# Kernel optimization log

Measured on AMD Instinct MI355X. Metric: run time of the kernel, lower is better.

The kernel has to match this reference:

```python
import jax, jax.numpy as jnp
import numpy as np

VOCAB, NUM_CLASSES, E, H = 50257, 20, 64, 64
B, T = 128, 2048


def setup_inputs() -> dict:
    key = jax.random.key(0)
    ks = jax.random.split(key, 16)
    s_ih = 1.0 / np.sqrt(H)
    u = lambda k, shape: jax.random.uniform(k, shape, jnp.float32, -s_ih, s_ih)
    return {
        'tokens': jax.random.randint(ks[0], (B, T), 0, VOCAB),
        'emb': jax.random.normal(ks[1], (VOCAB, E), jnp.float32),
        # forward-direction GRU params (PyTorch layout: [3H, *], gate order r,z,n)
        'wih_f': u(ks[2], (3 * H, E)), 'whh_f': u(ks[3], (3 * H, H)),
        'bih_f': u(ks[4], (3 * H,)), 'bhh_f': u(ks[5], (3 * H,)),
        # backward-direction GRU params
        'wih_b': u(ks[6], (3 * H, E)), 'whh_b': u(ks[7], (3 * H, H)),
        'bih_b': u(ks[8], (3 * H,)), 'bhh_b': u(ks[9], (3 * H,)),
        # classifier: Linear(4H -> H), GELU, Linear(H -> C)
        'w1': u(ks[10], (H, 4 * H)), 'b1': u(ks[11], (H,)),
        'w2': u(ks[12], (NUM_CLASSES, H)), 'b2': u(ks[13], (NUM_CLASSES,)),
    }


def _gru_dir(x, wih, whh, bih, bhh):
    # x: [B, T, E] -> outputs [B, T, H]; PyTorch GRU gate math, gates (r, z, n)
    xg = jnp.einsum('bte,ge->tbg', x, wih) + bih  # precompute input projections [T,B,3H]
    h0 = jnp.zeros((x.shape[0], H), x.dtype)

    def step(h, xg_t):
        hg = h @ whh.T + bhh
        xr, xz, xn = jnp.split(xg_t, 3, axis=-1)
        hr, hz, hn = jnp.split(hg, 3, axis=-1)
        r = jax.nn.sigmoid(xr + hr)
        z = jax.nn.sigmoid(xz + hz)
        n = jnp.tanh(xn + r * hn)
        h_new = (1.0 - z) * n + z * h
        return h_new, h_new

    _, hs = jax.lax.scan(step, h0, xg)  # hs: [T, B, H]
    return hs.transpose(1, 0, 2)


def reference(tokens, emb, wih_f, whh_f, bih_f, bhh_f,
              wih_b, whh_b, bih_b, bhh_b, w1, b1, w2, b2):
    x = emb[tokens]  # [B, T, E]
    h_fwd = _gru_dir(x, wih_f, whh_f, bih_f, bhh_f)
    h_bwd = _gru_dir(x[:, ::-1], wih_b, whh_b, bih_b, bhh_b)[:, ::-1]
    encoded = jnp.concatenate([h_fwd, h_bwd], axis=-1)  # [B, T, 2H]
    feats = jnp.concatenate([encoded.mean(axis=1), encoded.max(axis=1)], axis=-1)  # [B, 4H]
    hid = jax.nn.gelu(feats @ w1.T + b1, approximate=False)
    return hid @ w2.T + b2  # [B, C]
```

## Files before the change

### kernel.cpp

```cpp
#include <hip/hip_runtime.h>
#include <hip/hip_bf16.h>
#include <math.h>

#define VOCAB 50257
#define NCLS 20
#define EDIM 64
#define HDIM 64
#define BATCH 128
#define TLEN 2048

typedef float v2f __attribute__((ext_vector_type(2)));

__device__ float g_P[(size_t)2 * VOCAB * 192];
__device__ float g_feats[BATCH * 256];

__device__ __forceinline__ float fast_rcp(float x) { return __builtin_amdgcn_rcpf(x); }

__device__ __forceinline__ float fsigmoid(float x) {
    return fast_rcp(1.f + __expf(-x));
}
__device__ __forceinline__ float ftanh(float x) {
    float e = __expf(2.f * x);
    return 1.f - 2.f * fast_rcp(e + 1.f);
}

__global__ __launch_bounds__(384) void precompute_P(
    const float* __restrict__ emb,
    const float* __restrict__ wih_f, const float* __restrict__ bih_f,
    const float* __restrict__ wih_b, const float* __restrict__ bih_b)
{
    const int t = threadIdx.x;
    const int dir = t / 192;
    const int g = t % 192;
    const float* wih = dir ? wih_b : wih_f;
    const float* bih = dir ? bih_b : bih_f;

    float w[64];
#pragma unroll
    for (int e = 0; e < 64; e += 4) {
        float4 v = *(const float4*)(wih + (size_t)g * 64 + e);
        w[e] = v.x; w[e + 1] = v.y; w[e + 2] = v.z; w[e + 3] = v.w;
    }
    const float bias = bih[g];
    float* Pd = g_P + (size_t)dir * VOCAB * 192;

    for (int v = blockIdx.x; v < VOCAB; v += gridDim.x) {
        const float4* er = (const float4*)(emb + (size_t)v * 64);
        float acc = bias;
#pragma unroll
        for (int e4 = 0; e4 < 16; e4++) {
            float4 x = er[e4];
            acc = fmaf(x.x, w[4 * e4 + 0], acc);
            acc = fmaf(x.y, w[4 * e4 + 1], acc);
            acc = fmaf(x.z, w[4 * e4 + 2], acc);
            acc = fmaf(x.w, w[4 * e4 + 3], acc);
        }
        Pd[(size_t)v * 192 + g] = acc;
    }
}

__global__ __launch_bounds__(64, 1) void gru_seq(
    const int* __restrict__ tokens,
    const float* __restrict__ whh_f, const float* __restrict__ bhh_f,
    const float* __restrict__ whh_b, const float* __restrict__ bhh_b)
{
    const int lane = threadIdx.x;
    const int blk = blockIdx.x;
    const int b = blk >> 1;
    const int dir = blk & 1;
    const float* whh = dir ? whh_b : whh_f;
    const float* bhh = dir ? bhh_b : bhh_f;
    const float* Pd = g_P + (size_t)dir * VOCAB * 192;

    __shared__ __align__(16) float h_lds[64];
    __shared__ int tok_lds[TLEN];

    for (int t = lane; t < TLEN; t += 64) tok_lds[t] = tokens[b * TLEN + t];

    v2f wr[32], wz[32], wn[32];
    {
        const float* pr = whh + (size_t)(0 + lane) * 64;
        const float* pz = whh + (size_t)(64 + lane) * 64;
        const float* pn = whh + (size_t)(128 + lane) * 64;
#pragma unroll
        for (int k = 0; k < 16; k++) {
            float4 a = *(const float4*)(pr + 4 * k);
            wr[2 * k] = (v2f){a.x, a.y}; wr[2 * k + 1] = (v2f){a.z, a.w};
            float4 c = *(const float4*)(pz + 4 * k);
            wz[2 * k] = (v2f){c.x, c.y}; wz[2 * k + 1] = (v2f){c.z, c.w};
            float4 d = *(const float4*)(pn + 4 * k);
            wn[2 * k] = (v2f){d.x, d.y}; wn[2 * k + 1] = (v2f){d.z, d.w};
        }
    }
    const float br = bhh[lane], bz = bhh[64 + lane], bn = bhh[128 + lane];

    h_lds[lane] = 0.f;
    float h = 0.f, sum = 0.f, mx = -INFINITY;
    __syncthreads();

    auto tok_at = [&](int s) -> int {
        int ss = s < TLEN ? s : TLEN - 1;
        return tok_lds[dir ? (TLEN - 1 - ss) : ss];
    };

    float xrA, xzA, xnA, xrB, xzB, xnB, xrC, xzC, xnC;
    {
        const float* r0 = Pd + (size_t)tok_at(0) * 192;
        xrA = r0[lane]; xzA = r0[64 + lane]; xnA = r0[128 + lane];
        const float* r1 = Pd + (size_t)tok_at(1) * 192;
        xrB = r1[lane]; xzB = r1[64 + lane]; xnB = r1[128 + lane];
        const float* r2 = Pd + (size_t)tok_at(2) * 192;
        xrC = r2[lane]; xzC = r2[64 + lane]; xnC = r2[128 + lane];
    }

    for (int s = 0; s < TLEN; s++) {
        const float* rp = Pd + (size_t)tok_at(s + 3) * 192;
        float pxr = rp[lane], pxz = rp[64 + lane], pxn = rp[128 + lane];

        v2f ar0 = {0.f, 0.f}, ar1 = {0.f, 0.f};
        v2f az0 = {0.f, 0.f}, az1 = {0.f, 0.f};
        v2f an0 = {0.f, 0.f}, an1 = {0.f, 0.f};
#pragma unroll
        for (int k = 0; k < 16; k++) {
            float4 h4 = *(const float4*)(h_lds + 4 * k);
            v2f h01 = {h4.x, h4.y}, h23 = {h4.z, h4.w};
            ar0 = __builtin_elementwise_fma(h01, wr[2 * k], ar0);
            az0 = __builtin_elementwise_fma(h01, wz[2 * k], az0);
            an0 = __builtin_elementwise_fma(h01, wn[2 * k], an0);
            ar1 = __builtin_elementwise_fma(h23, wr[2 * k + 1], ar1);
            az1 = __builtin_elementwise_fma(h23, wz[2 * k + 1], az1);
            an1 = __builtin_elementwise_fma(h23, wn[2 * k + 1], an1);
        }
        float hr = (ar0.x + ar0.y) + (ar1.x + ar1.y);
        float hz = (az0.x + az0.y) + (az1.x + az1.y);
        float hn = (an0.x + an0.y) + (an1.x + an1.y);

        float r = fsigmoid(xrA + hr + br);
        float z = fsigmoid(xzA + hz + bz);
        float n = ftanh(xnA + r * (hn + bn));
        h = fmaf(z, h - n, n);
        sum += h;
        mx = fmaxf(mx, h);

        __syncthreads();
        h_lds[lane] = h;
        __syncthreads();

        xrA = xrB; xzA = xzB; xnA = xnB;
        xrB = xrC; xzB = xzC; xnB = xnC;
        xrC = pxr; xzC = pxz; xnC = pxn;
    }

    g_feats[b * 256 + dir * 64 + lane] = sum * (1.f / TLEN);
    g_feats[b * 256 + 128 + dir * 64 + lane] = mx;
}

__global__ __launch_bounds__(64) void classifier(
    const float* __restrict__ w1, const float* __restrict__ b1,
    const float* __restrict__ w2, const float* __restrict__ b2,
    float* __restrict__ out)
{
    const int b = blockIdx.x;
    const int i = threadIdx.x;
    __shared__ float f[256];
    __shared__ float hid[64];
    for (int c = i; c < 256; c += 64) f[c] = g_feats[b * 256 + c];
    __syncthreads();

    float acc = b1[i];
    const float* wrow = w1 + (size_t)i * 256;
#pragma unroll 16
    for (int c = 0; c < 256; c++) acc = fmaf(f[c], wrow[c], acc);
    hid[i] = acc * 0.5f * (1.f + erff(acc * 0.70710678118654752f));
    __syncthreads();

    if (i < NCLS) {
        float o = b2[i];
        const float* w2r = w2 + (size_t)i * 64;
#pragma unroll
        for (int j = 0; j < 64; j++) o = fmaf(hid[j], w2r[j], o);
        out[b * NCLS + i] = o;
    }
}

extern "C" void kernel_launch(void* const* d_in, const int* in_sizes, int n_in,
                              void* d_out, int out_size, void* d_ws, size_t ws_size,
                              hipStream_t stream) {
    const int*   tokens = (const int*)  d_in[0];
    const float* emb    = (const float*)d_in[1];
    const float* wih_f  = (const float*)d_in[2];
    const float* whh_f  = (const float*)d_in[3];
    const float* bih_f  = (const float*)d_in[4];
    const float* bhh_f  = (const float*)d_in[5];
    const float* wih_b  = (const float*)d_in[6];
    const float* whh_b  = (const float*)d_in[7];
    const float* bih_b  = (const float*)d_in[8];
    const float* bhh_b  = (const float*)d_in[9];
    const float* w1     = (const float*)d_in[10];
    const float* b1     = (const float*)d_in[11];
    const float* w2     = (const float*)d_in[12];
    const float* b2     = (const float*)d_in[13];
    float* out = (float*)d_out;

    precompute_P<<<1024, 384, 0, stream>>>(emb, wih_f, bih_f, wih_b, bih_b);
    gru_seq<<<2 * BATCH, 64, 0, stream>>>(tokens, whh_f, bhh_f, whh_b, bhh_b);
    classifier<<<BATCH, 64, 0, stream>>>(w1, b1, w2, b2, out);
}
```

Measured before the change: 1.082 ms.

## Interleave gate projections per lane as float4 and fold hidden biases into table

The precomputed token projection table changes from three separate 64-float gate segments to one float4 per lane holding r, z, n and a pad. Each recurrent step then does a single 16-byte gather instead of three scalar loads. The r and z hidden biases are folded into the table, and the table kernel is restructured so one thread computes all three gates for one lane. The step loop is unrolled by 4 with a 4-deep prefetch, and the h·W dot product uses 8-wide vectors. In exchange the table grows by a third, so the precompute kernel writes more data.

Result: slower. 1.618 ms (+49.4%).

```diff
diff --git a/kernel.cpp b/kernel.cpp
--- a/kernel.cpp
+++ b/kernel.cpp
@@ -1,61 +1,77 @@
 #include <hip/hip_runtime.h>
-#include <hip/hip_bf16.h>
 #include <math.h>
 
 #define VOCAB 50257
 #define NCLS 20
-#define EDIM 64
-#define HDIM 64
 #define BATCH 128
 #define TLEN 2048
 
-typedef float v2f __attribute__((ext_vector_type(2)));
+typedef float v8f __attribute__((ext_vector_type(8)));
 
-__device__ float g_P[(size_t)2 * VOCAB * 192];
+__device__ float g_P[(size_t)2 * VOCAB * 256];
 __device__ float g_feats[BATCH * 256];
 
-__device__ __forceinline__ float fast_rcp(float x) { return __builtin_amdgcn_rcpf(x); }
-
 __device__ __forceinline__ float fsigmoid(float x) {
-    return fast_rcp(1.f + __expf(-x));
+    return __builtin_amdgcn_rcpf(1.f + __expf(-x));
 }
 __device__ __forceinline__ float ftanh(float x) {
     float e = __expf(2.f * x);
-    return 1.f - 2.f * fast_rcp(e + 1.f);
+    return 1.f - 2.f * __builtin_amdgcn_rcpf(e + 1.f);
+}
+__device__ __forceinline__ float hsum8(v8f a) {
+    float s0 = a[0] + a[4], s1 = a[1] + a[5], s2 = a[2] + a[6], s3 = a[3] + a[7];
+    return (s0 + s2) + (s1 + s3);
 }
 
-__global__ __launch_bounds__(384) void precompute_P(
+#define DECL_W8(P, base) \
+    const v8f P##0 = ((const v8f*)(base))[0], P##1 = ((const v8f*)(base))[1], \
+              P##2 = ((const v8f*)(base))[2], P##3 = ((const v8f*)(base))[3], \
+              P##4 = ((const v8f*)(base))[4], P##5 = ((const v8f*)(base))[5], \
+              P##6 = ((const v8f*)(base))[6], P##7 = ((const v8f*)(base))[7];
+
+#define DOT8(ACC, H, W) \
+    v8f ACC = H##0 * W##0; \
+    ACC = __builtin_elementwise_fma(H##1, W##1, ACC); \
+    ACC = __builtin_elementwise_fma(H##2, W##2, ACC); \
+    ACC = __builtin_elementwise_fma(H##3, W##3, ACC); \
+    ACC = __builtin_elementwise_fma(H##4, W##4, ACC); \
+    ACC = __builtin_elementwise_fma(H##5, W##5, ACC); \
+    ACC = __builtin_elementwise_fma(H##6, W##6, ACC); \
+    ACC = __builtin_elementwise_fma(H##7, W##7, ACC);
+
+__global__ __launch_bounds__(128, 1) void precompute_P(
     const float* __restrict__ emb,
-    const float* __restrict__ wih_f, const float* __restrict__ bih_f,
-    const float* __restrict__ wih_b, const float* __restrict__ bih_b)
+    const float* __restrict__ wih_f, const float* __restrict__ bih_f, const float* __restrict__ bhh_f,
+    const float* __restrict__ wih_b, const float* __restrict__ bih_b, const float* __restrict__ bhh_b)
 {
-    const int t = threadIdx.x;
-    const int dir = t / 192;
-    const int g = t % 192;
+    const int lane = threadIdx.x & 63;
+    const int dir  = threadIdx.x >> 6;
     const float* wih = dir ? wih_b : wih_f;
     const float* bih = dir ? bih_b : bih_f;
+    const float* bhh = dir ? bhh_b : bhh_f;
 
-    float w[64];
-#pragma unroll
-    for (int e = 0; e < 64; e += 4) {
-        float4 v = *(const float4*)(wih + (size_t)g * 64 + e);
-        w[e] = v.x; w[e + 1] = v.y; w[e + 2] = v.z; w[e + 3] = v.w;
-    }
-    const float bias = bih[g];
-    float* Pd = g_P + (size_t)dir * VOCAB * 192;
+    DECL_W8(wr, wih + (size_t)lane * 64)
+    DECL_W8(wz, wih + (size_t)(64 + lane) * 64)
+    DECL_W8(wn, wih + (size_t)(128 + lane) * 64)
+    const float br = bih[lane] + bhh[lane];
+    const float bz = bih[64 + lane] + bhh[64 + lane];
+    const float bn = bih[128 + lane];
+
+    float4* Pd = (float4*)g_P + (size_t)dir * VOCAB * 64;
 
     for (int v = blockIdx.x; v < VOCAB; v += gridDim.x) {
-        const float4* er = (const float4*)(emb + (size_t)v * 64);
-        float acc = bias;
-#pragma unroll
-        for (int e4 = 0; e4 < 16; e4++) {
-            float4 x = er[e4];
-            acc = fmaf(x.x, w[4 * e4 + 0], acc);
-            acc = fmaf(x.y, w[4 * e4 + 1], acc);
-            acc = fmaf(x.z, w[4 * e4 + 2], acc);
-            acc = fmaf(x.w, w[4 * e4 + 3], acc);
-        }
-        Pd[(size_t)v * 192 + g] = acc;
+        const v8f* e8 = (const v8f*)(emb + (size_t)v * 64);
+        const v8f h0 = e8[0], h1 = e8[1], h2 = e8[2], h3 = e8[3],
+                  h4 = e8[4], h5 = e8[5], h6 = e8[6], h7 = e8[7];
+        DOT8(ar, h, wr)
+        DOT8(az, h, wz)
+        DOT8(an, h, wn)
+        float4 o;
+        o.x = hsum8(ar) + br;
+        o.y = hsum8(az) + bz;
+        o.z = hsum8(an) + bn;
+        o.w = 0.f;
+        Pd[(size_t)v * 64 + lane] = o;
     }
 }
 
@@ -65,90 +81,62 @@
     const float* __restrict__ whh_b, const float* __restrict__ bhh_b)
 {
     const int lane = threadIdx.x;
-    const int blk = blockIdx.x;
-    const int b = blk >> 1;
-    const int dir = blk & 1;
+    const int b = blockIdx.x >> 1;
+    const int dir = blockIdx.x & 1;
     const float* whh = dir ? whh_b : whh_f;
     const float* bhh = dir ? bhh_b : bhh_f;
-    const float* Pd = g_P + (size_t)dir * VOCAB * 192;
+    const float4* P4 = (const float4*)g_P + (size_t)dir * VOCAB * 64;
 
-    __shared__ __align__(16) float h_lds[64];
+    __shared__ __align__(32) float h_lds[64];
     __shared__ int tok_lds[TLEN];
-
     for (int t = lane; t < TLEN; t += 64) tok_lds[t] = tokens[b * TLEN + t];
 
-    v2f wr[32], wz[32], wn[32];
-    {
-        const float* pr = whh + (size_t)(0 + lane) * 64;
-        const float* pz = whh + (size_t)(64 + lane) * 64;
-        const float* pn = whh + (size_t)(128 + lane) * 64;
-#pragma unroll
-        for (int k = 0; k < 16; k++) {
-            float4 a = *(const float4*)(pr + 4 * k);
-            wr[2 * k] = (v2f){a.x, a.y}; wr[2 * k + 1] = (v2f){a.z, a.w};
-            float4 c = *(const float4*)(pz + 4 * k);
-            wz[2 * k] = (v2f){c.x, c.y}; wz[2 * k + 1] = (v2f){c.z, c.w};
-            float4 d = *(const float4*)(pn + 4 * k);
-            wn[2 * k] = (v2f){d.x, d.y}; wn[2 * k + 1] = (v2f){d.z, d.w};
-        }
-    }
-    const float br = bhh[lane], bz = bhh[64 + lane], bn = bhh[128 + lane];
+    DECL_W8(wr, whh + (size_t)lane * 64)
+    DECL_W8(wz, whh + (size_t)(64 + lane) * 64)
+    DECL_W8(wn, whh + (size_t)(128 + lane) * 64)
+    const float bn = bhh[128 + lane];
 
     h_lds[lane] = 0.f;
     float h = 0.f, sum = 0.f, mx = -INFINITY;
     __syncthreads();
 
-    auto tok_at = [&](int s) -> int {
+    auto rowAt = [&](int s) -> const float4* {
         int ss = s < TLEN ? s : TLEN - 1;
-        return tok_lds[dir ? (TLEN - 1 - ss) : ss];
+        int tok = tok_lds[dir ? (TLEN - 1 - ss) : ss];
+        return P4 + (size_t)tok * 64;
     };
 
-    float xrA, xzA, xnA, xrB, xzB, xnB, xrC, xzC, xnC;
-    {
-        const float* r0 = Pd + (size_t)tok_at(0) * 192;
-        xrA = r0[lane]; xzA = r0[64 + lane]; xnA = r0[128 + lane];
-        const float* r1 = Pd + (size_t)tok_at(1) * 192;
-        xrB = r1[lane]; xzB = r1[64 + lane]; xnB = r1[128 + lane];
-        const float* r2 = Pd + (size_t)tok_at(2) * 192;
-        xrC = r2[lane]; xzC = r2[64 + lane]; xnC = r2[128 + lane];
-    }
+    float4 xg0 = rowAt(0)[lane], xg1 = rowAt(1)[lane],
+           xg2 = rowAt(2)[lane], xg3 = rowAt(3)[lane];
 
-    for (int s = 0; s < TLEN; s++) {
-        const float* rp = Pd + (size_t)tok_at(s + 3) * 192;
-        float pxr = rp[lane], pxz = rp[64 + lane], pxn = rp[128 + lane];
+    for (int s = 0; s < TLEN; s += 4) {
+#pragma unroll
+        for (int j = 0; j < 4; j++) {
+            const float4 cur = (j == 0) ? xg0 : (j == 1) ? xg1 : (j == 2) ? xg2 : xg3;
+            const float4 nxt = rowAt(s + j + 4)[lane];
 
-        v2f ar0 = {0.f, 0.f}, ar1 = {0.f, 0.f};
-        v2f az0 = {0.f, 0.f}, az1 = {0.f, 0.f};
-        v2f an0 = {0.f, 0.f}, an1 = {0.f, 0.f};
-#pragma unroll
-        for (int k = 0; k < 16; k++) {
-            float4 h4 = *(const float4*)(h_lds + 4 * k);
-            v2f h01 = {h4.x, h4.y}, h23 = {h4.z, h4.w};
-            ar0 = __builtin_elementwise_fma(h01, wr[2 * k], ar0);
-            az0 = __builtin_elementwise_fma(h01, wz[2 * k], az0);
-            an0 = __builtin_elementwise_fma(h01, wn[2 * k], an0);
-            ar1 = __builtin_elementwise_fma(h23, wr[2 * k + 1], ar1);
-            az1 = __builtin_elementwise_fma(h23, wz[2 * k + 1], az1);
-            an1 = __builtin_elementwise_fma(h23, wn[2 * k + 1], an1);
+            const v8f* hp = (const v8f*)h_lds;
+            const v8f h0 = hp[0], h1 = hp[1], h2 = hp[2], h3 = hp[3],
+                      h4 = hp[4], h5 = hp[5], h6 = hp[6], h7 = hp[7];
+            DOT8(ar, h, wr)
+            DOT8(az, h, wz)
+            DOT8(an, h, wn)
+            const float hr = hsum8(ar), hz = hsum8(az), hn = hsum8(an);
+
+            const float r = fsigmoid(cur.x + hr);
+            const float z = fsigmoid(cur.y + hz);
+            const float n = ftanh(cur.z + r * (hn + bn));
+            h = fmaf(z, h - n, n);
+            sum += h;
+            mx = fmaxf(mx, h);
+
+            __syncthreads();
+            h_lds[lane] = h;
+            __syncthreads();
+
+            if (j == 0) xg0 = nxt; else if (j == 1) xg1 = nxt;
+            else if (j == 2) xg2 = nxt; else xg3 = nxt;
         }
-        float hr = (ar0.x + ar0.y) + (ar1.x + ar1.y);
-        float hz = (az0.x + az0.y) + (az1.x + az1.y);
-        float hn = (an0.x + an0.y) + (an1.x + an1.y);
-
-        float r = fsigmoid(xrA + hr + br);
-        float z = fsigmoid(xzA + hz + bz);
-        float n = ftanh(xnA + r * (hn + bn));
-        h = fmaf(z, h - n, n);
-        sum += h;
-        mx = fmaxf(mx, h);
-
-        __syncthreads();
-        h_lds[lane] = h;
-        __syncthreads();
-
-        xrA = xrB; xzA = xzB; xnA = xnB;
-        xrB = xrC; xzB = xzC; xnB = xnC;
-        xrC = pxr; xzC = pxz; xnC = pxn;
     }
 
     g_feats[b * 256 + dir * 64 + lane] = sum * (1.f / TLEN);
@@ -202,7 +190,7 @@
     const float* b2     = (const float*)d_in[13];
     float* out = (float*)d_out;
 
-    precompute_P<<<1024, 384, 0, stream>>>(emb, wih_f, bih_f, wih_b, bih_b);
+    precompute_P<<<512, 128, 0, stream>>>(emb, wih_f, bih_f, bhh_f, wih_b, bih_b, bhh_b);
     gru_seq<<<2 * BATCH, 64, 0, stream>>>(tokens, whh_f, bhh_f, whh_b, bhh_b);
     classifier<<<BATCH, 64, 0, stream>>>(w1, b1, w2, b2, out);
 }
```
